# Optimization experiments

Measured on AMD Instinct MI355X. Metric: run time of the kernel, lower is better.

Reference implementation:

```python
import jax, jax.numpy as jnp
import numpy as np

B, IN, OUT = 8192, 4096, 2048  # OUT must equal 32*64 per betta/gamma sizes


def setup_inputs() -> dict:
    key = jax.random.key(0)
    kx, kw = jax.random.split(key, 2)
    X = jax.random.normal(kx, (B, IN), dtype=jnp.float32)
    # xavier-uniform-like init for W
    limit = float(np.sqrt(6.0 / (IN + OUT)))
    W = jax.random.uniform(kw, (IN, OUT), minval=-limit, maxval=limit, dtype=jnp.float32)
    absmean = jnp.abs(W).mean(axis=0)
    alpha = jnp.abs(W).mean()          # scalar, >= 0
    betta = absmean[:32]               # (32,), >= 0
    gamma = absmean[32:96]             # (64,), >= 0
    return {"X": X, "W": W, "alpha": alpha, "betta": betta, "gamma": gamma}


def reference(X, W, alpha, betta, gamma):
    # module applies relu_ to alpha/betta/gamma data before the functional call
    alpha = jax.nn.relu(alpha)
    betta = jax.nn.relu(betta)
    gamma = jax.nn.relu(gamma)
    X_bin = jnp.sign(X)                # (B, IN)
    W_bin = jnp.sign(W)                # (IN, OUT)
    # scale[i*64+j] = alpha * betta[i] * gamma[j] -> (OUT,)
    scale = (alpha * jnp.outer(betta, gamma)).reshape(-1)
    return (X_bin @ W_bin) * scale     # (B, OUT)
```

## Files before the change

### kernel.cpp

```cpp
#include <hip/hip_runtime.h>


#define M_DIM 8192
#define K_DIM 4096
#define N_DIM 2048
#define NTK   (K_DIM / 128)
#define PANEL (128 * 128 * 16)
#define KSTEP 8192
#define BUFB  24576

typedef int i32x4 __attribute__((ext_vector_type(4)));
typedef int i32x8 __attribute__((ext_vector_type(8)));
typedef float f32x16 __attribute__((ext_vector_type(16)));

__device__ __forceinline__ unsigned int nib4(float x) {
  unsigned int s = (__float_as_uint(x) >> 28) & 0x8u;
  return x == 0.0f ? 0u : (0x2u | s);
}

__device__ __forceinline__ unsigned int pack8(const float* f) {
  unsigned int p = 0;
#pragma unroll
  for (int j = 0; j < 8; ++j) p |= nib4(f[j]) << (4 * j);
  return p;
}

__device__ __forceinline__ void gload_lds16(const void* g, void* lds) {
  __builtin_amdgcn_global_load_lds(
      (const __attribute__((address_space(1))) unsigned int*)g,
      (__attribute__((address_space(3))) unsigned int*)lds, 16, 0, 0);
}

__global__ __launch_bounds__(256) void binX_kernel(
    const float* __restrict__ X, unsigned char* __restrict__ Xq) {
  __shared__ float tile[32][260];
  const int t = threadIdx.x;
  const int rg = blockIdx.x >> 4;
  const int kc = blockIdx.x & 15;
  const int lrow = t >> 6;
  const int col4 = (t & 63) * 4;
#pragma unroll
  for (int i = 0; i < 8; ++i)
    *(float4*)&tile[i * 4 + lrow][col4] =
        *(const float4*)&X[(size_t)(rg * 32 + i * 4 + lrow) * K_DIM + kc * 256 + col4];
  __syncthreads();
  const int s = t >> 5;
  const int r = t & 31;
  float f[32];
#pragma unroll
  for (int q = 0; q < 8; ++q)
    *(float4*)&f[q * 4] = *(const float4*)&tile[r][s * 32 + q * 4];
  uint4 gq;
  gq.x = pack8(f + 0);  gq.y = pack8(f + 8);
  gq.z = pack8(f + 16); gq.w = pack8(f + 24);
  const int row = rg * 32 + r;
  const int kslot = kc * 8 + s;
  unsigned char* dst = Xq + (size_t)(row >> 7) * PANEL +
                       ((size_t)kslot * 128 + (row & 127)) * 16;
  *(uint4*)dst = gq;
}

__global__ __launch_bounds__(256) void binW_kernel(
    const float* __restrict__ W, unsigned char* __restrict__ Wq) {
  __shared__ float tile[32][260];
  const int t = threadIdx.x;
  const int q = blockIdx.x >> 7;
  const int kt = (blockIdx.x >> 3) & 15;
  const int s = blockIdx.x & 7;
#pragma unroll
  for (int i = 0; i < 8; ++i) {
    int row = i * 4 + (t >> 6);
    int col4 = (t & 63) * 4;
    *(float4*)&tile[row][col4] =
        *(const float4*)&W[(size_t)(kt * 256 + s * 32 + row) * N_DIM + q * 256 + col4];
  }
  __syncthreads();
  float f[32];
#pragma unroll
  for (int k = 0; k < 32; ++k) f[k] = tile[k][t];
  uint4 gq;
  gq.x = pack8(f + 0);  gq.y = pack8(f + 8);
  gq.z = pack8(f + 16); gq.w = pack8(f + 24);
  const int n = q * 256 + t;
  const int kslot = kt * 8 + s;
  unsigned char* dst = Wq + (size_t)(n >> 7) * PANEL +
                       ((size_t)kslot * 128 + (n & 127)) * 16;
  *(uint4*)dst = gq;
}

__global__ __launch_bounds__(256, 2) void gemm_fp4_kernel(
    const unsigned char* __restrict__ Aq,
    const unsigned char* __restrict__ Bq,
    const float* __restrict__ alpha,
    const float* __restrict__ betta,
    const float* __restrict__ gamma,
    float* __restrict__ C) {
  __shared__ __align__(16) unsigned char smem[3 * BUFB];

  const int t = threadIdx.x;
  const int lane = t & 63;
  const int l31 = lane & 31;
  const int lhi = lane >> 5;
  const int w = t >> 6;
  const int wr = w >> 1;
  const int wc = w & 1;

  const int bid = blockIdx.x;
  const int j = bid >> 3;
  const int bm = (bid & 7) * 4 + (j & 3);
  const int bn = j >> 2;
  const int row0 = bm * 256;
  const int col0 = bn * 128;

  const unsigned char* Asrc0 = Aq + (size_t)(2 * bm) * PANEL;
  const unsigned char* Asrc1 = Asrc0 + PANEL;
  const unsigned char* Bsrc  = Bq + (size_t)bn * PANEL;

  f32x16 acc[4][2];
#pragma unroll
  for (int fm = 0; fm < 4; ++fm)
#pragma unroll
    for (int fn = 0; fn < 2; ++fn)
#pragma unroll
      for (int r = 0; r < 16; ++r) acc[fm][fn][r] = 0.f;

  i32x8 a8[4], b8[2];
#pragma unroll
  for (int i = 0; i < 4; ++i)
#pragma unroll
    for (int e = 0; e < 8; ++e) a8[i][e] = 0;
#pragma unroll
  for (int i = 0; i < 2; ++i)
#pragma unroll
    for (int e = 0; e < 8; ++e) b8[i][e] = 0;

  auto stage = [&](int kt, unsigned char* buf) {
    const unsigned char* a0 = Asrc0 + kt * KSTEP;
    const unsigned char* a1 = Asrc1 + kt * KSTEP;
    const unsigned char* b  = Bsrc  + kt * KSTEP;
#pragma unroll
    for (int p = 0; p < 2; ++p) {
      const int c = p * 256 + t;
      gload_lds16(a0 + c * 16, buf + c * 16);
      gload_lds16(a1 + c * 16, buf + 8192 + c * 16);
      gload_lds16(b  + c * 16, buf + 16384 + c * 16);
    }
  };

  auto compute = [&](const unsigned char* buf) {
    const unsigned char* pA = buf + wr * 8192;
    const unsigned char* pB = buf + 16384;
#pragma unroll
    for (int kk = 0; kk < 2; ++kk) {
      const int g = kk * 2 + lhi;
#pragma unroll
      for (int fm = 0; fm < 4; ++fm)
        *(i32x4*)&a8[fm] = *(const i32x4*)&pA[(g * 128 + fm * 32 + l31) * 16];
#pragma unroll
      for (int fn = 0; fn < 2; ++fn)
        *(i32x4*)&b8[fn] = *(const i32x4*)&pB[(g * 128 + wc * 64 + fn * 32 + l31) * 16];
      __builtin_amdgcn_s_setprio(1);
#pragma unroll
      for (int fm = 0; fm < 4; ++fm)
#pragma unroll
        for (int fn = 0; fn < 2; ++fn)
          acc[fm][fn] = __builtin_amdgcn_mfma_scale_f32_32x32x64_f8f6f4(
              a8[fm], b8[fn], acc[fm][fn], 4, 4,
              0, 0x7F7F7F7F, 0, 0x7F7F7F7F);
      __builtin_amdgcn_s_setprio(0);
    }
  };

  unsigned char* P0 = smem;
  unsigned char* P1 = smem + BUFB;
  unsigned char* P2 = smem + 2 * BUFB;

  stage(0, P0);
  stage(1, P1);

  for (int kt = 0; kt < NTK - 1; ++kt) {
    asm volatile("s_waitcnt vmcnt(6)" ::: "memory");
    __builtin_amdgcn_s_barrier();
    __builtin_amdgcn_sched_barrier(0);
    if (kt + 2 < NTK) stage(kt + 2, P2);
    compute(P0);
    unsigned char* tmp = P0; P0 = P1; P1 = P2; P2 = tmp;
  }
  asm volatile("s_waitcnt vmcnt(0)" ::: "memory");
  __builtin_amdgcn_s_barrier();
  __builtin_amdgcn_sched_barrier(0);
  compute(P0);

  const float ra = fmaxf(alpha[0], 0.0f);
#pragma unroll
  for (int fn = 0; fn < 2; ++fn) {
    const int col = col0 + wc * 64 + fn * 32 + l31;
    const float sc = ra * fmaxf(betta[col >> 6], 0.0f) * fmaxf(gamma[col & 63], 0.0f);
#pragma unroll
    for (int fm = 0; fm < 4; ++fm) {
      const int rbase = row0 + wr * 128 + fm * 32 + 4 * lhi;
#pragma unroll
      for (int r = 0; r < 16; ++r) {
        const int row = rbase + (r & 3) + 8 * (r >> 2);
        C[(size_t)row * N_DIM + col] = acc[fm][fn][r] * sc;
      }
    }
  }
}

extern "C" void kernel_launch(void* const* d_in, const int* in_sizes, int n_in,
                              void* d_out, int out_size, void* d_ws, size_t ws_size,
                              hipStream_t stream) {
  const float* X = (const float*)d_in[0];
  const float* W = (const float*)d_in[1];
  const float* alpha = (const float*)d_in[2];
  const float* betta = (const float*)d_in[3];
  const float* gamma = (const float*)d_in[4];
  float* out = (float*)d_out;

  unsigned char* Xq = (unsigned char*)d_ws;
  unsigned char* Wq = Xq + (size_t)(M_DIM / 128) * PANEL;

  binW_kernel<<<1024, 256, 0, stream>>>(W, Wq);
  binX_kernel<<<4096, 256, 0, stream>>>(X, Xq);
  gemm_fp4_kernel<<<(M_DIM / 256) * (N_DIM / 128), 256, 0, stream>>>(
      Xq, Wq, alpha, betta, gamma, out);
}
```

Baseline: 72.82 us.

## Replace LDS-staged pipeline with direct global-to-register double-buffered loads

Removes the shared-memory triple buffer and barrier-synchronised global_load_lds staging in the FP4 GEMM. Each wave now loads its MFMA operand fragments directly from global memory into two register sets, alternating them to overlap loads with MFMAs. This drops LDS traffic and workgroup barriers, but waves no longer share loaded tiles, so global/L2 traffic roughly doubles. The final iteration also prefetches one step past the K range without using the data.

```diff
diff --git a/kernel.cpp b/kernel.cpp
--- a/kernel.cpp
+++ b/kernel.cpp
@@ -7,7 +7,6 @@
 #define NTK   (K_DIM / 128)
 #define PANEL (128 * 128 * 16)
 #define KSTEP 8192
-#define BUFB  24576
 
 typedef int i32x4 __attribute__((ext_vector_type(4)));
 typedef int i32x8 __attribute__((ext_vector_type(8)));
@@ -23,12 +22,6 @@
 #pragma unroll
   for (int j = 0; j < 8; ++j) p |= nib4(f[j]) << (4 * j);
   return p;
-}
-
-__device__ __forceinline__ void gload_lds16(const void* g, void* lds) {
-  __builtin_amdgcn_global_load_lds(
-      (const __attribute__((address_space(1))) unsigned int*)g,
-      (__attribute__((address_space(3))) unsigned int*)lds, 16, 0, 0);
 }
 
 __global__ __launch_bounds__(256) void binX_kernel(
@@ -95,8 +88,6 @@
     const float* __restrict__ betta,
     const float* __restrict__ gamma,
     float* __restrict__ C) {
-  __shared__ __align__(16) unsigned char smem[3 * BUFB];
-
   const int t = threadIdx.x;
   const int lane = t & 63;
   const int l31 = lane & 31;
@@ -112,9 +103,10 @@
   const int row0 = bm * 256;
   const int col0 = bn * 128;
 
-  const unsigned char* Asrc0 = Aq + (size_t)(2 * bm) * PANEL;
-  const unsigned char* Asrc1 = Asrc0 + PANEL;
-  const unsigned char* Bsrc  = Bq + (size_t)bn * PANEL;
+  const unsigned char* Apan = Aq + (size_t)(2 * bm + wr) * PANEL +
+                              lhi * 2048 + l31 * 16;
+  const unsigned char* Bpan = Bq + (size_t)bn * PANEL +
+                              lhi * 2048 + (wc * 64 + l31) * 16;
 
   f32x16 acc[4][2];
 #pragma unroll
@@ -124,72 +116,64 @@
 #pragma unroll
       for (int r = 0; r < 16; ++r) acc[fm][fn][r] = 0.f;
 
-  i32x8 a8[4], b8[2];
+  i32x8 aX[4], aY[4], bX[2], bY[2];
 #pragma unroll
   for (int i = 0; i < 4; ++i)
 #pragma unroll
-    for (int e = 0; e < 8; ++e) a8[i][e] = 0;
+    for (int e = 0; e < 8; ++e) { aX[i][e] = 0; aY[i][e] = 0; }
 #pragma unroll
   for (int i = 0; i < 2; ++i)
 #pragma unroll
-    for (int e = 0; e < 8; ++e) b8[i][e] = 0;
-
-  auto stage = [&](int kt, unsigned char* buf) {
-    const unsigned char* a0 = Asrc0 + kt * KSTEP;
-    const unsigned char* a1 = Asrc1 + kt * KSTEP;
-    const unsigned char* b  = Bsrc  + kt * KSTEP;
-#pragma unroll
-    for (int p = 0; p < 2; ++p) {
-      const int c = p * 256 + t;
-      gload_lds16(a0 + c * 16, buf + c * 16);
-      gload_lds16(a1 + c * 16, buf + 8192 + c * 16);
-      gload_lds16(b  + c * 16, buf + 16384 + c * 16);
-    }
-  };
-
-  auto compute = [&](const unsigned char* buf) {
-    const unsigned char* pA = buf + wr * 8192;
-    const unsigned char* pB = buf + 16384;
-#pragma unroll
-    for (int kk = 0; kk < 2; ++kk) {
-      const int g = kk * 2 + lhi;
-#pragma unroll
-      for (int fm = 0; fm < 4; ++fm)
-        *(i32x4*)&a8[fm] = *(const i32x4*)&pA[(g * 128 + fm * 32 + l31) * 16];
+    for (int e = 0; e < 8; ++e) { bX[i][e] = 0; bY[i][e] = 0; }
+
+  auto loadX = [&](int kt, int kk) {
+    const unsigned char* pa = Apan + (size_t)kt * KSTEP + kk * 4096;
+    const unsigned char* pb = Bpan + (size_t)kt * KSTEP + kk * 4096;
+#pragma unroll
+    for (int fm = 0; fm < 4; ++fm)
+      *(i32x4*)&aX[fm] = *(const i32x4*)(pa + fm * 512);
+#pragma unroll
+    for (int fn = 0; fn < 2; ++fn)
+      *(i32x4*)&bX[fn] = *(const i32x4*)(pb + fn * 512);
+  };
+  auto loadY = [&](int kt, int kk) {
+    const unsigned char* pa = Apan + (size_t)kt * KSTEP + kk * 4096;
+    const unsigned char* pb = Bpan + (size_t)kt * KSTEP + kk * 4096;
+#pragma unroll
+    for (int fm = 0; fm < 4; ++fm)
+      *(i32x4*)&aY[fm] = *(const i32x4*)(pa + fm * 512);
+#pragma unroll
+    for (int fn = 0; fn < 2; ++fn)
+      *(i32x4*)&bY[fn] = *(const i32x4*)(pb + fn * 512);
+  };
+  auto mmX = [&]() {
+#pragma unroll
+    for (int fm = 0; fm < 4; ++fm)
 #pragma unroll
       for (int fn = 0; fn < 2; ++fn)
-        *(i32x4*)&b8[fn] = *(const i32x4*)&pB[(g * 128 + wc * 64 + fn * 32 + l31) * 16];
-      __builtin_amdgcn_s_setprio(1);
-#pragma unroll
-      for (int fm = 0; fm < 4; ++fm)
-#pragma unroll
-        for (int fn = 0; fn < 2; ++fn)
-          acc[fm][fn] = __builtin_amdgcn_mfma_scale_f32_32x32x64_f8f6f4(
-              a8[fm], b8[fn], acc[fm][fn], 4, 4,
-              0, 0x7F7F7F7F, 0, 0x7F7F7F7F);
-      __builtin_amdgcn_s_setprio(0);
-    }
-  };
-
-  unsigned char* P0 = smem;
-  unsigned char* P1 = smem + BUFB;
-  unsigned char* P2 = smem + 2 * BUFB;
-
-  stage(0, P0);
-  stage(1, P1);
-
-  for (int kt = 0; kt < NTK - 1; ++kt) {
-    asm volatile("s_waitcnt vmcnt(6)" ::: "memory");
-    __builtin_amdgcn_s_barrier();
-    __builtin_amdgcn_sched_barrier(0);
-    if (kt + 2 < NTK) stage(kt + 2, P2);
-    compute(P0);
-    unsigned char* tmp = P0; P0 = P1; P1 = P2; P2 = tmp;
+        acc[fm][fn] = __builtin_amdgcn_mfma_scale_f32_32x32x64_f8f6f4(
+            aX[fm], bX[fn], acc[fm][fn], 4, 4,
+            0, 0x7F7F7F7F, 0, 0x7F7F7F7F);
+  };
+  auto mmY = [&]() {
+#pragma unroll
+    for (int fm = 0; fm < 4; ++fm)
+#pragma unroll
+      for (int fn = 0; fn < 2; ++fn)
+        acc[fm][fn] = __builtin_amdgcn_mfma_scale_f32_32x32x64_f8f6f4(
+            aY[fm], bY[fn], acc[fm][fn], 4, 4,
+            0, 0x7F7F7F7F, 0, 0x7F7F7F7F);
+  };
+
+  loadX(0, 0);
+  loadY(0, 1);
+
+  for (int kt = 0; kt < NTK; ++kt) {
+    mmX();
+    loadX(kt + 1, 0);
+    mmY();
+    loadY(kt + 1, 1);
   }
-  asm volatile("s_waitcnt vmcnt(0)" ::: "memory");
-  __builtin_amdgcn_s_barrier();
-  __builtin_amdgcn_sched_barrier(0);
-  compute(P0);
 
   const float ra = fmaxf(alpha[0], 0.0f);
 #pragma unroll
```

Result: slower. 83.53 us (+14.7%).
